# Optimization experiments

Hardware: AMD Instinct MI355X
Metric: run time of the kernel (lower is better)

Reference implementation:

```python
import jax, jax.numpy as jnp
import numpy as np

DT = 0.1
B_SZ = 8192
T_HIST = 20
LEN_PRED = 30
FEAT = 32
N_LAYERS = 3
# state transition for constant-acceleration model (matches self.F in torch)
F_MAT = np.array([[1.0, DT, DT * DT / 2], [0.0, 1.0, DT], [0.0, 0.0, 1.0]], dtype=np.float32)


def setup_inputs() -> dict:
    key = jax.random.key(0)
    ks = jax.random.split(key, 16)
    # random-walk trajectories as history observations
    hist = jnp.cumsum(jax.random.normal(ks[0], (B_SZ, T_HIST, 2), jnp.float32) * 0.5, axis=1)
    k_lin = 1.0 / np.sqrt(FEAT)
    k_in = 1.0 / np.sqrt(24)

    def u(k, shape, scale):
        return jax.random.uniform(k, shape, jnp.float32, -scale, scale)

    return {
        "hist": hist,
        "max_accel_x": jnp.ones((1,), jnp.float32) * 10.0,
        "max_accel_y": jnp.ones((1,), jnp.float32) * 20.0,
        "velocity_std_x": jnp.ones((1,), jnp.float32) * 10.0,
        "acceleration_std_x": jnp.ones((1,), jnp.float32) * 10.0,
        "R_x_": jnp.array([0.0448], jnp.float32),
        "R_y_": jnp.array([0.001], jnp.float32),
        "G_x": jnp.array([0.0059, 0.2981, 0.0393], jnp.float32),
        "G_y": jnp.array([0.0059, 0.2981, 0.0393], jnp.float32) / 5.0,
        "Win_W": u(ks[1], (FEAT, 24), k_in),
        "Win_b": u(ks[2], (FEAT,), k_in),
        "enc_Wih": u(ks[3], (N_LAYERS, 4 * FEAT, FEAT), k_lin),
        "enc_Whh": u(ks[4], (N_LAYERS, 4 * FEAT, FEAT), k_lin),
        "enc_bih": u(ks[5], (N_LAYERS, 4 * FEAT), k_lin),
        "enc_bhh": u(ks[6], (N_LAYERS, 4 * FEAT), k_lin),
        "dec_Wih": u(ks[7], (N_LAYERS, 4 * FEAT, FEAT), k_lin),
        "dec_Whh": u(ks[8], (N_LAYERS, 4 * FEAT, FEAT), k_lin),
        "dec_bih": u(ks[9], (N_LAYERS, 4 * FEAT), k_lin),
        "dec_bhh": u(ks[10], (N_LAYERS, 4 * FEAT), k_lin),
        "Wout_W": u(ks[11], (4, FEAT), k_lin),
        "Wout_b": u(ks[12], (4,), k_lin),
        "len_pred": LEN_PRED,
    }


def reference(hist, max_accel_x, max_accel_y, velocity_std_x, acceleration_std_x,
              R_x_, R_y_, G_x, G_y, Win_W, Win_b,
              enc_Wih, enc_Whh, enc_bih, enc_bhh,
              dec_Wih, dec_Whh, dec_bih, dec_bhh,
              Wout_W, Wout_b, len_pred):
    B = hist.shape[0]
    F = jnp.asarray(F_MAT)
    R_x = R_x_[0] * R_x_[0]
    R_y = R_y_[0] * R_y_[0]
    Z_x = hist[:, :, 0]
    Z_y = hist[:, :, 1]

    def lstm(x, h, c, Wih, Whh, bih, bhh):
        g = x @ Wih.T + bih + h @ Whh.T + bhh
        i, f, gg, o = jnp.split(g, 4, axis=1)
        c = jax.nn.sigmoid(f) * c + jax.nn.sigmoid(i) * jnp.tanh(gg)
        h = jax.nn.sigmoid(o) * jnp.tanh(c)
        return h, c

    def stack(XP, h, c, Wih, Whh, bih, bhh):
        x = jnp.tanh(XP @ Win_W.T + Win_b)
        hs, cs = [], []
        for j in range(N_LAYERS):
            hj, cj = lstm(x, h[j], c[j], Wih[j], Whh[j], bih[j], bhh[j])
            hs.append(hj)
            cs.append(cj)
            x = cj  # torch code feeds the fresh CELL state to the next layer
        return jnp.stack(hs), jnp.stack(cs)

    def kpred(X, P, Q):
        return X @ F.T, jnp.einsum('ij,bjk,lk->bil', F, P, F) + Q

    def kupdate(X, P, z, R):
        y = z - X[:, 0]                      # innovation (H picks component 0)
        S = P[:, 0, 0] + R                   # innovation covariance (scalar)
        K = P[:, :, 0] / S[:, None]          # Kalman gain (B,3)
        return X + y[:, None] * K, P - K[:, :, None] * P[:, 0:1, :]

    def kinit(z0):
        # torch always calls _kalman_init with is_x=True (default), so both
        # axes use R_x / velocity_std_x / acceleration_std_x
        X = jnp.zeros((B, 3), hist.dtype).at[:, 0].set(z0)
        d = jnp.stack([R_x, velocity_std_x[0] ** 2, acceleration_std_x[0] ** 2])
        P = jnp.zeros((B, 3, 3), hist.dtype).at[:, jnp.arange(3), jnp.arange(3)].set(d)
        return X, P

    Qx_e = jnp.outer(G_x * max_accel_x[0], G_x * max_accel_x[0])
    Qy_e = jnp.outer(G_y * max_accel_y[0], G_y * max_accel_y[0])

    Xx, Px = kinit(Z_x[:, 0])
    Xy, Py = kinit(Z_y[:, 0])
    h = jnp.zeros((N_LAYERS, B, FEAT), hist.dtype)
    c = jnp.zeros_like(h)

    def enc_step(carry, zs):
        Xx, Px, Xy, Py, h, c = carry
        zx, zy = zs
        XP = jnp.concatenate([Xx, Xy, Px.reshape(B, 9), Py.reshape(B, 9)], 1)
        h, c = stack(XP, h, c, enc_Wih, enc_Whh, enc_bih, enc_bhh)
        Xx, Px = kpred(Xx, Px, Qx_e)
        Xy, Py = kpred(Xy, Py, Qy_e)
        Xx, Px = kupdate(Xx, Px, zx, R_x)
        Xy, Py = kupdate(Xy, Py, zy, R_y)
        return (Xx, Px, Xy, Py, h, c), None

    carry, _ = jax.lax.scan(enc_step, (Xx, Px, Xy, Py, h, c),
                            (Z_x[:, 1:].T, Z_y[:, 1:].T))

    oxx = jnp.outer(G_x, G_x)
    oyy = jnp.outer(G_y, G_y)

    def dec_step(carry, _):
        Xx, Px, Xy, Py, h, c = carry
        XP = jnp.concatenate([Xx, Xy, Px.reshape(B, 9), Py.reshape(B, 9)], 1)
        h, c = stack(XP, h, c, dec_Wih, dec_Whh, dec_bih, dec_bhh)
        pred = c[-1] @ Wout_W.T + Wout_b  # (B,4): [u_x, u_y, std_x, std_y]
        Xx = Xx.at[:, 2].set(DT * pred[:, 0])  # X[:,2] = B*u
        Xy = Xy.at[:, 2].set(DT * pred[:, 1])
        Qx = (pred[:, 2] ** 2)[:, None, None] * oxx
        Qy = (pred[:, 3] ** 2)[:, None, None] * oyy
        Xx, Px = kpred(Xx, Px, Qx)
        Xy, Py = kpred(Xy, Py, Qy)
        out = jnp.stack([Xx[:, 0], Xy[:, 0],
                         jnp.sqrt(Px[:, 0, 0]), jnp.sqrt(Py[:, 0, 0]),
                         jnp.zeros(B, hist.dtype)], axis=1)  # (B,5)
        return (Xx, Px, Xy, Py, h, c), out

    carry, ys = jax.lax.scan(dec_step, carry, None, length=len_pred)
    return jnp.transpose(ys, (1, 0, 2))  # (B, len_pred, 5)
```

## Files before the change

kernel.cpp:

```cpp
#include <hip/hip_runtime.h>
#include <math.h>

#define DT   0.1f
#define HDT  0.005f
#define T_HIST 20
#define LEN_PRED 30

typedef __attribute__((ext_vector_type(8))) short bfrag8;
typedef __attribute__((ext_vector_type(4))) short short4v;
typedef __attribute__((ext_vector_type(4))) float f32x4;

#define WS_FRAG   0u
#define WS_WIN    98304u
#define WS_WOUT   100352u
#define WS_BIAS   101376u

static __device__ __forceinline__ unsigned short f2bf(float x) {
    union { float f; unsigned int u; } v; v.f = x;
    unsigned int r = v.u + 0x7fffu + ((v.u >> 16) & 1u);
    return (unsigned short)(r >> 16);
}

__global__ void prep_kernel(const float* __restrict__ Win_W,
                            const float* __restrict__ eWih, const float* __restrict__ eWhh,
                            const float* __restrict__ ebih, const float* __restrict__ ebhh,
                            const float* __restrict__ dWih, const float* __restrict__ dWhh,
                            const float* __restrict__ dbih, const float* __restrict__ dbhh,
                            const float* __restrict__ Wout_W,
                            char* __restrict__ ws)
{
    int i = blockIdx.x * blockDim.x + threadIdx.x;
    if (i < 49152) {
        int fi = i >> 9, within = i & 511;
        int lane = within >> 3, jj = within & 7;
        int c = fi & 1, j = (fi >> 1) & 1, wvv = (fi >> 2) & 3;
        int pl = fi >> 4;
        int l = pl % 3, ph = pl / 3;
        int m = lane & 15, q2 = lane >> 4;
        int gate = m & 3;
        int feat = wvv * 8 + 4 * j + (m >> 2);
        int row = gate * 32 + feat;
        int k = q2 * 8 + jj;
        const float* W = (c == 0) ? (ph ? dWih : eWih) : (ph ? dWhh : eWhh);
        ((unsigned short*)(ws + WS_FRAG))[i] = f2bf(W[l * 4096 + row * 32 + k]);
    } else if (i < 50176) {
        int i2 = i - 49152;
        int w = i2 >> 9, within = i2 & 511;
        int lane = within >> 3, jj = within & 7;
        int m = lane & 15, q2 = lane >> 4;
        int k = q2 * 8 + jj;
        float v = (k < 24) ? Win_W[(w * 16 + m) * 24 + k] : 0.f;
        ((unsigned short*)(ws + WS_WIN))[i2] = f2bf(v);
    } else if (i < 50688) {
        int i3 = i - 50176;
        int lane = i3 >> 3, jj = i3 & 7;
        int m = lane & 15, q2 = lane >> 4;
        float v = (m < 4) ? Wout_W[m * 32 + q2 * 8 + jj] : 0.f;
        ((unsigned short*)(ws + WS_WOUT))[i3] = f2bf(v);
    } else if (i < 51456) {
        int b = i - 50688;
        int ph = b / 384, rem = b % 384;
        int l = rem >> 7, row = rem & 127;
        const float* bi = ph ? dbih : ebih;
        const float* bh = ph ? dbhh : ebhh;
        ((float*)(ws + WS_BIAS))[b] = bi[l * 128 + row] + bh[l * 128 + row];
    }
}

__launch_bounds__(256, 2)
__global__ void kalman_lstm_kernel(const float* __restrict__ hist,
                                   const float* __restrict__ max_ax, const float* __restrict__ max_ay,
                                   const float* __restrict__ vstd, const float* __restrict__ astd,
                                   const float* __restrict__ Rx_, const float* __restrict__ Ry_,
                                   const float* __restrict__ Gx, const float* __restrict__ Gy,
                                   const float* __restrict__ Win_b, const float* __restrict__ Wout_b,
                                   const char* __restrict__ ws, float* __restrict__ out)
{
    __shared__ __align__(16) unsigned short xin[4][16][40];
    __shared__ __align__(16) unsigned short hbuf[2][3][16][40];
    __shared__ __align__(16) unsigned short xpw[2][16][40];

    const int tid  = threadIdx.x;
    const int wv   = tid >> 6;
    const int lane = tid & 63;
    const int q    = lane >> 4;
    const int m    = lane & 15;
    const int b_elem = blockIdx.x * 16 + m;

    bfrag8 fragA[3][2][2];
    float  biasR[3][2][4];
    const bfrag8* fragp = (const bfrag8*)(ws + WS_FRAG);
    const float*  combp = (const float*)(ws + WS_BIAS);
    auto load_phase = [&](int ph) {
#pragma unroll
        for (int l = 0; l < 3; ++l)
#pragma unroll
            for (int j = 0; j < 2; ++j) {
#pragma unroll
                for (int c = 0; c < 2; ++c) {
                    int fi = (((ph * 3 + l) * 4 + wv) * 2 + j) * 2 + c;
                    fragA[l][j][c] = fragp[fi * 64 + lane];
                }
#pragma unroll
                for (int r = 0; r < 4; ++r)
                    biasR[l][j][r] = combp[ph * 384 + l * 128 + r * 32 + (wv * 8 + 4 * j + q)];
            }
    };
    load_phase(0);

    bfrag8 winF = {}, woutF = {};
    f32x4 winB = {0.f, 0.f, 0.f, 0.f};
    float wb0 = 0.f, wb1 = 0.f, wb2 = 0.f, wb3 = 0.f;
    float g0 = 0.f, g1 = 0.f, g2 = 0.f, ge0 = 0.f, ge1 = 0.f, ge2 = 0.f;
    float Rch = 0.f, X0 = 0.f, X1 = 0.f, X2 = 0.f;
    float P00 = 0.f, P01 = 0.f, P02 = 0.f, P11 = 0.f, P12 = 0.f, P22 = 0.f;
    const int ch = q & 1;
    if (wv >= 2) {
        int w = wv - 2;
        winF  = ((const bfrag8*)(ws + WS_WIN))[w * 64 + lane];
        woutF = ((const bfrag8*)(ws + WS_WOUT))[lane];
#pragma unroll
        for (int r = 0; r < 4; ++r) winB[r] = Win_b[w * 16 + q * 4 + r];
        wb0 = Wout_b[0]; wb1 = Wout_b[1]; wb2 = Wout_b[2]; wb3 = Wout_b[3];
        const float rx = Rx_[0] * Rx_[0], ry = Ry_[0] * Ry_[0];
        Rch = ch ? ry : rx;
        if (ch == 0) { g0 = Gx[0]; g1 = Gx[1]; g2 = Gx[2]; float s = max_ax[0]; ge0 = g0*s; ge1 = g1*s; ge2 = g2*s; }
        else         { g0 = Gy[0]; g1 = Gy[1]; g2 = Gy[2]; float s = max_ay[0]; ge0 = g0*s; ge1 = g1*s; ge2 = g2*s; }
        X0 = hist[b_elem * (T_HIST * 2) + ch];
        P00 = Rch; P11 = vstd[0] * vstd[0]; P22 = astd[0] * astd[0];
    }

    float creg[3][2];
#pragma unroll
    for (int l = 0; l < 3; ++l) { creg[l][0] = 0.f; creg[l][1] = 0.f; }

    for (int idx = tid; idx < 4 * 16 * 40; idx += 256) (&xin[0][0][0])[idx] = 0;
    for (int idx = tid; idx < 2 * 3 * 16 * 40; idx += 256) (&hbuf[0][0][0][0])[idx] = 0;
    for (int idx = tid; idx < 2 * 16 * 40; idx += 256) (&xpw[0][0][0])[idx] = 0;

    auto sig = [](float z) { return __builtin_amdgcn_rcpf(1.f + __expf(-z)); };
    auto th  = [](float z) { return fmaf(-2.f, __builtin_amdgcn_rcpf(__expf(2.f * z) + 1.f), 1.f); };

    auto kpred = [&](float Q00, float Q01, float Q02, float Q11, float Q12, float Q22) {
        X0 = X0 + DT * X1 + HDT * X2;
        X1 = X1 + DT * X2;
        float M00 = P00 + DT * P01 + HDT * P02;
        float M01 = P01 + DT * P11 + HDT * P12;
        float M02 = P02 + DT * P12 + HDT * P22;
        float M11 = P11 + DT * P12;
        float M12 = P12 + DT * P22;
        float M22 = P22;
        P00 = M00 + DT * M01 + HDT * M02 + Q00;
        P01 = M01 + DT * M02 + Q01;
        P02 = M02 + Q02;
        P11 = M11 + DT * M12 + Q11;
        P12 = M12 + Q12;
        P22 = M22 + Q22;
    };
    auto kupdate = [&](float z) {
        float y = z - X0;
        float Sinv = 1.0f / (P00 + Rch);
        float K0 = P00 * Sinv, K1 = P01 * Sinv, K2 = P02 * Sinv;
        X0 += y * K0; X1 += y * K1; X2 += y * K2;
        float p00 = P00, p01 = P01, p02 = P02;
        P00 = p00 - K0 * p00;
        P01 = p01 - K0 * p01;
        P02 = p02 - K0 * p02;
        P11 = P11 - K1 * p01;
        P12 = P12 - K1 * p02;
        P22 = P22 - K2 * p02;
    };
    auto write_xp = [&]() {
        if (q < 2) {
            unsigned short* row = &xpw[wv - 2][m][0];
            int o = ch * 3;
            row[o + 0] = f2bf(X0); row[o + 1] = f2bf(X1); row[o + 2] = f2bf(X2);
            int pb = 6 + ch * 9;
            row[pb + 0] = f2bf(P00); row[pb + 1] = f2bf(P01); row[pb + 2] = f2bf(P02);
            row[pb + 3] = f2bf(P01); row[pb + 4] = f2bf(P11); row[pb + 5] = f2bf(P12);
            row[pb + 6] = f2bf(P02); row[pb + 7] = f2bf(P12); row[pb + 8] = f2bf(P22);
        }
    };

    const f32x4 zero4 = {0.f, 0.f, 0.f, 0.f};

    auto regionA = [&](int mode, int t) {
        if (wv >= 2) {
            if (mode == 0) {
                if (t > 0) {
                    float z = hist[b_elem * (T_HIST * 2) + t * 2 + ch];
                    kpred(ge0 * ge0, ge0 * ge1, ge0 * ge2, ge1 * ge1, ge1 * ge2, ge2 * ge2);
                    kupdate(z);
                }
            } else {
                if (t == 0) {
                    float z = hist[b_elem * (T_HIST * 2) + 19 * 2 + ch];
                    kpred(ge0 * ge0, ge0 * ge1, ge0 * ge2, ge1 * ge1, ge1 * ge2, ge2 * ge2);
                    kupdate(z);
                } else {
                    bfrag8 bc2 = *(const bfrag8*)&xin[3][m][q * 8];
                    f32x4 ap = __builtin_amdgcn_mfma_f32_16x16x32_bf16(woutF, bc2, zero4, 0, 0, 0);
                    float a0 = ap[0] + wb0, a1 = ap[1] + wb1, a2 = ap[2] + wb2, a3 = ap[3] + wb3;
                    float s0 = __shfl(a0, m), s1 = __shfl(a1, m);
                    float s2 = __shfl(a2, m), s3 = __shfl(a3, m);
                    float pe = ch ? s1 : s0;
                    float qe = ch ? s3 : s2;
                    X2 = DT * pe;
                    float qs = qe * qe;
                    kpred(qs*g0*g0, qs*g0*g1, qs*g0*g2, qs*g1*g1, qs*g1*g2, qs*g2*g2);
                    if (wv == 2 && q < 2) {
                        float* o = out + (size_t)b_elem * (LEN_PRED * 5) + (t - 1) * 5;
                        if (ch == 0) { o[0] = X0; o[2] = sqrtf(P00); }
                        else         { o[1] = X0; o[3] = sqrtf(P00); o[4] = 0.f; }
                    }
                }
            }
            write_xp();
            bfrag8 bxp = *(const bfrag8*)&xpw[wv - 2][m][q * 8];
            f32x4 aw = __builtin_amdgcn_mfma_f32_16x16x32_bf16(winF, bxp, zero4, 0, 0, 0);
            union { short4v v; unsigned short s[4]; } u;
#pragma unroll
            for (int r = 0; r < 4; ++r) u.s[r] = f2bf(th(aw[r] + winB[r]));
            *(short4v*)&xin[0][m][(wv - 2) * 16 + q * 4] = u.v;
        }
        __syncthreads();
    };

    auto layers = [&](int p) {
#pragma unroll
        for (int l = 0; l < 3; ++l) {
            bfrag8 bx = *(const bfrag8*)&xin[l][m][q * 8];
            bfrag8 bh = *(const bfrag8*)&hbuf[p][l][m][q * 8];
            f32x4 a0 = __builtin_amdgcn_mfma_f32_16x16x32_bf16(fragA[l][0][0], bx, zero4, 0, 0, 0);
            a0        = __builtin_amdgcn_mfma_f32_16x16x32_bf16(fragA[l][0][1], bh, a0, 0, 0, 0);
            f32x4 a1 = __builtin_amdgcn_mfma_f32_16x16x32_bf16(fragA[l][1][0], bx, zero4, 0, 0, 0);
            a1        = __builtin_amdgcn_mfma_f32_16x16x32_bf16(fragA[l][1][1], bh, a1, 0, 0, 0);
#pragma unroll
            for (int j = 0; j < 2; ++j) {
                f32x4 a = j ? a1 : a0;
                float iv = sig(a[0] + biasR[l][j][0]);
                float fv = sig(a[1] + biasR[l][j][1]);
                float gv = th (a[2] + biasR[l][j][2]);
                float ov = sig(a[3] + biasR[l][j][3]);
                float cn = fmaf(fv, creg[l][j], iv * gv);
                float hn = ov * th(cn);
                creg[l][j] = cn;
                int f = wv * 8 + 4 * j + q;
                xin[l + 1][m][f] = f2bf(cn);
                hbuf[p ^ 1][l][m][f] = f2bf(hn);
            }
            __syncthreads();
        }
    };

    __syncthreads();
    int p = 0;

    for (int t = 0; t < T_HIST - 1; ++t) { regionA(0, t); layers(p); p ^= 1; }
    load_phase(1);
    for (int t = 0; t < LEN_PRED; ++t)   { regionA(1, t); layers(p); p ^= 1; }

    if (wv == 2) {
        bfrag8 bc2 = *(const bfrag8*)&xin[3][m][q * 8];
        f32x4 ap = __builtin_amdgcn_mfma_f32_16x16x32_bf16(woutF, bc2, zero4, 0, 0, 0);
        float a0 = ap[0] + wb0, a1 = ap[1] + wb1, a2 = ap[2] + wb2, a3 = ap[3] + wb3;
        float s0 = __shfl(a0, m), s1 = __shfl(a1, m);
        float s2 = __shfl(a2, m), s3 = __shfl(a3, m);
        float pe = ch ? s1 : s0;
        float qe = ch ? s3 : s2;
        X2 = DT * pe;
        float qs = qe * qe;
        kpred(qs*g0*g0, qs*g0*g1, qs*g0*g2, qs*g1*g1, qs*g1*g2, qs*g2*g2);
        if (q < 2) {
            float* o = out + (size_t)b_elem * (LEN_PRED * 5) + (LEN_PRED - 1) * 5;
            if (ch == 0) { o[0] = X0; o[2] = sqrtf(P00); }
            else         { o[1] = X0; o[3] = sqrtf(P00); o[4] = 0.f; }
        }
    }
}

extern "C" void kernel_launch(void* const* d_in, const int* in_sizes, int n_in,
                              void* d_out, int out_size, void* d_ws, size_t ws_size,
                              hipStream_t stream)
{
    const float* hist  = (const float*)d_in[0];
    const float* maxax = (const float*)d_in[1];
    const float* maxay = (const float*)d_in[2];
    const float* vstd  = (const float*)d_in[3];
    const float* astd  = (const float*)d_in[4];
    const float* Rx    = (const float*)d_in[5];
    const float* Ry    = (const float*)d_in[6];
    const float* Gx    = (const float*)d_in[7];
    const float* Gy    = (const float*)d_in[8];
    const float* WinW  = (const float*)d_in[9];
    const float* Winb  = (const float*)d_in[10];
    const float* eWih  = (const float*)d_in[11];
    const float* eWhh  = (const float*)d_in[12];
    const float* ebih  = (const float*)d_in[13];
    const float* ebhh  = (const float*)d_in[14];
    const float* dWih  = (const float*)d_in[15];
    const float* dWhh  = (const float*)d_in[16];
    const float* dbih  = (const float*)d_in[17];
    const float* dbhh  = (const float*)d_in[18];
    const float* WoutW = (const float*)d_in[19];
    const float* Woutb = (const float*)d_in[20];
    char* ws = (char*)d_ws;
    float* out = (float*)d_out;

    prep_kernel<<<202, 256, 0, stream>>>(WinW, eWih, eWhh, ebih, ebhh,
                                         dWih, dWhh, dbih, dbhh, WoutW, ws);
    kalman_lstm_kernel<<<512, 256, 0, stream>>>(hist, maxax, maxay, vstd, astd,
                                                Rx, Ry, Gx, Gy, Winb, Woutb,
                                                ws, out);
}
```

Baseline: 192.8 us.

## Precompute encoder Kalman inputs, issue recurrent MFMAs early, repack LDS layout

Runs the whole encoder-phase Kalman filter and input projection up front, since it does not depend on the LSTM, and stages all 19 projected inputs in shared memory. This removes one barrier-separated region per encoder step. Each step now issues the hidden-state MFMAs for all layers first, with the bias folded into the accumulator, so they overlap the dependent chain. The shared buffers are changed to a k-chunked [4][16][8] layout with gate rows permuted, so each lane writes packed bf16 pairs via v_cvt_pk_bf16_f32. The trade-off is more shared memory, which may affect occupancy, and more live accumulator registers.

```diff
diff --git a/kernel.cpp b/kernel.cpp
--- a/kernel.cpp
+++ b/kernel.cpp
@@ -7,8 +7,8 @@
 #define LEN_PRED 30
 
 typedef __attribute__((ext_vector_type(8))) short bfrag8;
-typedef __attribute__((ext_vector_type(4))) short short4v;
 typedef __attribute__((ext_vector_type(4))) float f32x4;
+typedef __attribute__((ext_vector_type(2))) unsigned int u32x2;
 
 #define WS_FRAG   0u
 #define WS_WIN    98304u
@@ -19,6 +19,12 @@
     union { float f; unsigned int u; } v; v.f = x;
     unsigned int r = v.u + 0x7fffu + ((v.u >> 16) & 1u);
     return (unsigned short)(r >> 16);
+}
+
+static __device__ __forceinline__ unsigned int cvtpk(float lo, float hi) {
+    unsigned int r;
+    asm("v_cvt_pk_bf16_f32 %0, %1, %2" : "=v"(r) : "v"(lo), "v"(hi));
+    return r;
 }
 
 __global__ void prep_kernel(const float* __restrict__ Win_W,
@@ -36,9 +42,9 @@
         int c = fi & 1, j = (fi >> 1) & 1, wvv = (fi >> 2) & 3;
         int pl = fi >> 4;
         int l = pl % 3, ph = pl / 3;
-        int m = lane & 15, q2 = lane >> 4;
-        int gate = m & 3;
-        int feat = wvv * 8 + 4 * j + (m >> 2);
+        int p = lane & 15, q2 = lane >> 4;
+        int gate = p & 3;
+        int feat = wvv * 8 + (p >> 2) * 2 + j;
         int row = gate * 32 + feat;
         int k = q2 * 8 + jj;
         const float* W = (c == 0) ? (ph ? dWih : eWih) : (ph ? dWhh : eWhh);
@@ -47,15 +53,15 @@
         int i2 = i - 49152;
         int w = i2 >> 9, within = i2 & 511;
         int lane = within >> 3, jj = within & 7;
-        int m = lane & 15, q2 = lane >> 4;
+        int p = lane & 15, q2 = lane >> 4;
         int k = q2 * 8 + jj;
-        float v = (k < 24) ? Win_W[(w * 16 + m) * 24 + k] : 0.f;
+        float v = (k < 24) ? Win_W[(w * 16 + p) * 24 + k] : 0.f;
         ((unsigned short*)(ws + WS_WIN))[i2] = f2bf(v);
     } else if (i < 50688) {
         int i3 = i - 50176;
         int lane = i3 >> 3, jj = i3 & 7;
-        int m = lane & 15, q2 = lane >> 4;
-        float v = (m < 4) ? Wout_W[m * 32 + q2 * 8 + jj] : 0.f;
+        int p = lane & 15, q2 = lane >> 4;
+        float v = (p < 4) ? Wout_W[p * 32 + q2 * 8 + jj] : 0.f;
         ((unsigned short*)(ws + WS_WOUT))[i3] = f2bf(v);
     } else if (i < 51456) {
         int b = i - 50688;
@@ -76,9 +82,11 @@
                                    const float* __restrict__ Win_b, const float* __restrict__ Wout_b,
                                    const char* __restrict__ ws, float* __restrict__ out)
 {
-    __shared__ __align__(16) unsigned short xin[4][16][40];
-    __shared__ __align__(16) unsigned short hbuf[2][3][16][40];
-    __shared__ __align__(16) unsigned short xpw[2][16][40];
+    __shared__ __align__(16) unsigned short xin[4][4][16][8];
+    __shared__ __align__(16) unsigned short hbuf[2][3][4][16][8];
+    __shared__ __align__(16) unsigned short xpw[2][4][16][8];
+    __shared__ __align__(16) unsigned short xenc[T_HIST - 1][4][16][8];
+    __shared__ __align__(16) unsigned short xps[2][4][16][8];
 
     const int tid  = threadIdx.x;
     const int wv   = tid >> 6;
@@ -86,9 +94,10 @@
     const int q    = lane >> 4;
     const int m    = lane & 15;
     const int b_elem = blockIdx.x * 16 + m;
+    const f32x4 zero4 = {0.f, 0.f, 0.f, 0.f};
 
     bfrag8 fragA[3][2][2];
-    float  biasR[3][2][4];
+    f32x4  biasV[3][2];
     const bfrag8* fragp = (const bfrag8*)(ws + WS_FRAG);
     const float*  combp = (const float*)(ws + WS_BIAS);
     auto load_phase = [&](int ph) {
@@ -103,7 +112,7 @@
                 }
 #pragma unroll
                 for (int r = 0; r < 4; ++r)
-                    biasR[l][j][r] = combp[ph * 384 + l * 128 + r * 32 + (wv * 8 + 4 * j + q)];
+                    biasV[l][j][r] = combp[ph * 384 + l * 128 + r * 32 + (wv * 8 + q * 2 + j)];
             }
     };
     load_phase(0);
@@ -111,7 +120,8 @@
     bfrag8 winF = {}, woutF = {};
     f32x4 winB = {0.f, 0.f, 0.f, 0.f};
     float wb0 = 0.f, wb1 = 0.f, wb2 = 0.f, wb3 = 0.f;
-    float g0 = 0.f, g1 = 0.f, g2 = 0.f, ge0 = 0.f, ge1 = 0.f, ge2 = 0.f;
+    float g00 = 0.f, g01 = 0.f, g02 = 0.f, g11 = 0.f, g12 = 0.f, g22 = 0.f;
+    float qe00 = 0.f, qe01 = 0.f, qe02 = 0.f, qe11 = 0.f, qe12 = 0.f, qe22 = 0.f;
     float Rch = 0.f, X0 = 0.f, X1 = 0.f, X2 = 0.f;
     float P00 = 0.f, P01 = 0.f, P02 = 0.f, P11 = 0.f, P12 = 0.f, P22 = 0.f;
     const int ch = q & 1;
@@ -124,19 +134,25 @@
         wb0 = Wout_b[0]; wb1 = Wout_b[1]; wb2 = Wout_b[2]; wb3 = Wout_b[3];
         const float rx = Rx_[0] * Rx_[0], ry = Ry_[0] * Ry_[0];
         Rch = ch ? ry : rx;
-        if (ch == 0) { g0 = Gx[0]; g1 = Gx[1]; g2 = Gx[2]; float s = max_ax[0]; ge0 = g0*s; ge1 = g1*s; ge2 = g2*s; }
-        else         { g0 = Gy[0]; g1 = Gy[1]; g2 = Gy[2]; float s = max_ay[0]; ge0 = g0*s; ge1 = g1*s; ge2 = g2*s; }
+        float G0, G1, G2, sc;
+        if (ch == 0) { G0 = Gx[0]; G1 = Gx[1]; G2 = Gx[2]; sc = max_ax[0]; }
+        else         { G0 = Gy[0]; G1 = Gy[1]; G2 = Gy[2]; sc = max_ay[0]; }
+        g00 = G0 * G0; g01 = G0 * G1; g02 = G0 * G2;
+        g11 = G1 * G1; g12 = G1 * G2; g22 = G2 * G2;
+        float s2 = sc * sc;
+        qe00 = g00 * s2; qe01 = g01 * s2; qe02 = g02 * s2;
+        qe11 = g11 * s2; qe12 = g12 * s2; qe22 = g22 * s2;
         X0 = hist[b_elem * (T_HIST * 2) + ch];
-        P00 = Rch; P11 = vstd[0] * vstd[0]; P22 = astd[0] * astd[0];
+        P00 = rx; P11 = vstd[0] * vstd[0]; P22 = astd[0] * astd[0];
     }
 
     float creg[3][2];
 #pragma unroll
     for (int l = 0; l < 3; ++l) { creg[l][0] = 0.f; creg[l][1] = 0.f; }
 
-    for (int idx = tid; idx < 4 * 16 * 40; idx += 256) (&xin[0][0][0])[idx] = 0;
-    for (int idx = tid; idx < 2 * 3 * 16 * 40; idx += 256) (&hbuf[0][0][0][0])[idx] = 0;
-    for (int idx = tid; idx < 2 * 16 * 40; idx += 256) (&xpw[0][0][0])[idx] = 0;
+    for (int idx = tid; idx < 4 * 4 * 16 * 8; idx += 256) (&xin[0][0][0][0])[idx] = 0;
+    for (int idx = tid; idx < 2 * 3 * 4 * 16 * 8; idx += 256) (&hbuf[0][0][0][0][0])[idx] = 0;
+    for (int idx = tid; idx < 2 * 4 * 16 * 8; idx += 256) (&xpw[0][0][0][0])[idx] = 0;
 
     auto sig = [](float z) { return __builtin_amdgcn_rcpf(1.f + __expf(-z)); };
     auto th  = [](float z) { return fmaf(-2.f, __builtin_amdgcn_rcpf(__expf(2.f * z) + 1.f), 1.f); };
@@ -170,98 +186,131 @@
         P12 = P12 - K1 * p02;
         P22 = P22 - K2 * p02;
     };
-    auto write_xp = [&]() {
+    auto stage_xp = [&](unsigned short (*buf)[16][8]) {
         if (q < 2) {
-            unsigned short* row = &xpw[wv - 2][m][0];
+            auto wr = [&](int f, float v) { buf[f >> 3][m][f & 7] = f2bf(v); };
             int o = ch * 3;
-            row[o + 0] = f2bf(X0); row[o + 1] = f2bf(X1); row[o + 2] = f2bf(X2);
+            wr(o + 0, X0); wr(o + 1, X1); wr(o + 2, X2);
             int pb = 6 + ch * 9;
-            row[pb + 0] = f2bf(P00); row[pb + 1] = f2bf(P01); row[pb + 2] = f2bf(P02);
-            row[pb + 3] = f2bf(P01); row[pb + 4] = f2bf(P11); row[pb + 5] = f2bf(P12);
-            row[pb + 6] = f2bf(P02); row[pb + 7] = f2bf(P12); row[pb + 8] = f2bf(P22);
-        }
-    };
-
-    const f32x4 zero4 = {0.f, 0.f, 0.f, 0.f};
-
-    auto regionA = [&](int mode, int t) {
+            wr(pb + 0, P00); wr(pb + 1, P01); wr(pb + 2, P02);
+            wr(pb + 3, P01); wr(pb + 4, P11); wr(pb + 5, P12);
+            wr(pb + 6, P02); wr(pb + 7, P12); wr(pb + 8, P22);
+        }
+    };
+
+    auto gates = [&](int l, int pw, f32x4 a0, f32x4 a1) {
+        float i0 = sig(a0[0]), f0 = sig(a0[1]), gg0 = th(a0[2]), o0 = sig(a0[3]);
+        float c0 = fmaf(f0, creg[l][0], i0 * gg0);
+        float h0 = o0 * th(c0);
+        creg[l][0] = c0;
+        float i1 = sig(a1[0]), f1 = sig(a1[1]), gg1 = th(a1[2]), o1 = sig(a1[3]);
+        float c1 = fmaf(f1, creg[l][1], i1 * gg1);
+        float h1 = o1 * th(c1);
+        creg[l][1] = c1;
+        *(unsigned int*)&xin[l + 1][wv][m][q * 2]    = cvtpk(c0, c1);
+        *(unsigned int*)&hbuf[pw][l][wv][m][q * 2]   = cvtpk(h0, h1);
+    };
+
+    if (wv >= 2) {
+        const int w = wv - 2;
+        for (int idx = lane; idx < 4 * 16 * 8; idx += 64) (&xps[w][0][0][0])[idx] = 0;
+#pragma unroll 1
+        for (int s = 0; s < T_HIST - 1; ++s) {
+            if (s > 0) {
+                float z = hist[b_elem * (T_HIST * 2) + s * 2 + ch];
+                kpred(qe00, qe01, qe02, qe11, qe12, qe22);
+                kupdate(z);
+            }
+            stage_xp(xps[w]);
+            bfrag8 bxp = *(const bfrag8*)&xps[w][q][m][0];
+            f32x4 aw = __builtin_amdgcn_mfma_f32_16x16x32_bf16(winF, bxp, zero4, 0, 0, 0);
+            float v0 = th(aw[0] + winB[0]), v1 = th(aw[1] + winB[1]);
+            float v2 = th(aw[2] + winB[2]), v3 = th(aw[3] + winB[3]);
+            u32x2 pk; pk.x = cvtpk(v0, v1); pk.y = cvtpk(v2, v3);
+            *(u32x2*)&xenc[s][w * 2 + (q >> 1)][m][(q & 1) * 4] = pk;
+        }
+        {
+            float z = hist[b_elem * (T_HIST * 2) + 19 * 2 + ch];
+            kpred(qe00, qe01, qe02, qe11, qe12, qe22);
+            kupdate(z);
+        }
+    }
+    __syncthreads();
+
+    int p = 0;
+
+    for (int t = 0; t < T_HIST - 1; ++t) {
+        f32x4 ah[3][2];
+#pragma unroll
+        for (int l = 0; l < 3; ++l) {
+            bfrag8 bh = *(const bfrag8*)&hbuf[p][l][q][m][0];
+            ah[l][0] = __builtin_amdgcn_mfma_f32_16x16x32_bf16(fragA[l][0][1], bh, biasV[l][0], 0, 0, 0);
+            ah[l][1] = __builtin_amdgcn_mfma_f32_16x16x32_bf16(fragA[l][1][1], bh, biasV[l][1], 0, 0, 0);
+        }
+#pragma unroll
+        for (int l = 0; l < 3; ++l) {
+            bfrag8 bx = (l == 0) ? *(const bfrag8*)&xenc[t][q][m][0]
+                                 : *(const bfrag8*)&xin[l][q][m][0];
+            f32x4 a0 = __builtin_amdgcn_mfma_f32_16x16x32_bf16(fragA[l][0][0], bx, ah[l][0], 0, 0, 0);
+            f32x4 a1 = __builtin_amdgcn_mfma_f32_16x16x32_bf16(fragA[l][1][0], bx, ah[l][1], 0, 0, 0);
+            gates(l, p ^ 1, a0, a1);
+            __syncthreads();
+        }
+        p ^= 1;
+    }
+
+    load_phase(1);
+
+    for (int t = 0; t < LEN_PRED; ++t) {
+        bfrag8 bc2;
+        if (wv >= 2 && t > 0) bc2 = *(const bfrag8*)&xin[3][q][m][0];
+        f32x4 ah[3][2];
+#pragma unroll
+        for (int l = 0; l < 3; ++l) {
+            bfrag8 bh = *(const bfrag8*)&hbuf[p][l][q][m][0];
+            ah[l][0] = __builtin_amdgcn_mfma_f32_16x16x32_bf16(fragA[l][0][1], bh, biasV[l][0], 0, 0, 0);
+            ah[l][1] = __builtin_amdgcn_mfma_f32_16x16x32_bf16(fragA[l][1][1], bh, biasV[l][1], 0, 0, 0);
+        }
         if (wv >= 2) {
-            if (mode == 0) {
-                if (t > 0) {
-                    float z = hist[b_elem * (T_HIST * 2) + t * 2 + ch];
-                    kpred(ge0 * ge0, ge0 * ge1, ge0 * ge2, ge1 * ge1, ge1 * ge2, ge2 * ge2);
-                    kupdate(z);
-                }
-            } else {
-                if (t == 0) {
-                    float z = hist[b_elem * (T_HIST * 2) + 19 * 2 + ch];
-                    kpred(ge0 * ge0, ge0 * ge1, ge0 * ge2, ge1 * ge1, ge1 * ge2, ge2 * ge2);
-                    kupdate(z);
-                } else {
-                    bfrag8 bc2 = *(const bfrag8*)&xin[3][m][q * 8];
-                    f32x4 ap = __builtin_amdgcn_mfma_f32_16x16x32_bf16(woutF, bc2, zero4, 0, 0, 0);
-                    float a0 = ap[0] + wb0, a1 = ap[1] + wb1, a2 = ap[2] + wb2, a3 = ap[3] + wb3;
-                    float s0 = __shfl(a0, m), s1 = __shfl(a1, m);
-                    float s2 = __shfl(a2, m), s3 = __shfl(a3, m);
-                    float pe = ch ? s1 : s0;
-                    float qe = ch ? s3 : s2;
-                    X2 = DT * pe;
-                    float qs = qe * qe;
-                    kpred(qs*g0*g0, qs*g0*g1, qs*g0*g2, qs*g1*g1, qs*g1*g2, qs*g2*g2);
-                    if (wv == 2 && q < 2) {
-                        float* o = out + (size_t)b_elem * (LEN_PRED * 5) + (t - 1) * 5;
-                        if (ch == 0) { o[0] = X0; o[2] = sqrtf(P00); }
-                        else         { o[1] = X0; o[3] = sqrtf(P00); o[4] = 0.f; }
-                    }
+            const int w = wv - 2;
+            if (t > 0) {
+                f32x4 ap = __builtin_amdgcn_mfma_f32_16x16x32_bf16(woutF, bc2, zero4, 0, 0, 0);
+                float a0 = ap[0] + wb0, a1 = ap[1] + wb1, a2 = ap[2] + wb2, a3 = ap[3] + wb3;
+                float s0 = __shfl(a0, m), s1 = __shfl(a1, m);
+                float s2 = __shfl(a2, m), s3 = __shfl(a3, m);
+                float pe = ch ? s1 : s0;
+                float qe = ch ? s3 : s2;
+                X2 = DT * pe;
+                float qs = qe * qe;
+                kpred(qs * g00, qs * g01, qs * g02, qs * g11, qs * g12, qs * g22);
+                if (wv == 2 && q < 2) {
+                    float* o = out + (size_t)b_elem * (LEN_PRED * 5) + (t - 1) * 5;
+                    if (ch == 0) { o[0] = X0; o[2] = sqrtf(P00); }
+                    else         { o[1] = X0; o[3] = sqrtf(P00); o[4] = 0.f; }
                 }
             }
-            write_xp();
-            bfrag8 bxp = *(const bfrag8*)&xpw[wv - 2][m][q * 8];
+            stage_xp(xpw[w]);
+            bfrag8 bxp = *(const bfrag8*)&xpw[w][q][m][0];
             f32x4 aw = __builtin_amdgcn_mfma_f32_16x16x32_bf16(winF, bxp, zero4, 0, 0, 0);
-            union { short4v v; unsigned short s[4]; } u;
-#pragma unroll
-            for (int r = 0; r < 4; ++r) u.s[r] = f2bf(th(aw[r] + winB[r]));
-            *(short4v*)&xin[0][m][(wv - 2) * 16 + q * 4] = u.v;
+            float v0 = th(aw[0] + winB[0]), v1 = th(aw[1] + winB[1]);
+            float v2 = th(aw[2] + winB[2]), v3 = th(aw[3] + winB[3]);
+            u32x2 pk; pk.x = cvtpk(v0, v1); pk.y = cvtpk(v2, v3);
+            *(u32x2*)&xin[0][w * 2 + (q >> 1)][m][(q & 1) * 4] = pk;
         }
         __syncthreads();
-    };
-
-    auto layers = [&](int p) {
 #pragma unroll
         for (int l = 0; l < 3; ++l) {
-            bfrag8 bx = *(const bfrag8*)&xin[l][m][q * 8];
-            bfrag8 bh = *(const bfrag8*)&hbuf[p][l][m][q * 8];
-            f32x4 a0 = __builtin_amdgcn_mfma_f32_16x16x32_bf16(fragA[l][0][0], bx, zero4, 0, 0, 0);
-            a0        = __builtin_amdgcn_mfma_f32_16x16x32_bf16(fragA[l][0][1], bh, a0, 0, 0, 0);
-            f32x4 a1 = __builtin_amdgcn_mfma_f32_16x16x32_bf16(fragA[l][1][0], bx, zero4, 0, 0, 0);
-            a1        = __builtin_amdgcn_mfma_f32_16x16x32_bf16(fragA[l][1][1], bh, a1, 0, 0, 0);
-#pragma unroll
-            for (int j = 0; j < 2; ++j) {
-                f32x4 a = j ? a1 : a0;
-                float iv = sig(a[0] + biasR[l][j][0]);
-                float fv = sig(a[1] + biasR[l][j][1]);
-                float gv = th (a[2] + biasR[l][j][2]);
-                float ov = sig(a[3] + biasR[l][j][3]);
-                float cn = fmaf(fv, creg[l][j], iv * gv);
-                float hn = ov * th(cn);
-                creg[l][j] = cn;
-                int f = wv * 8 + 4 * j + q;
-                xin[l + 1][m][f] = f2bf(cn);
-                hbuf[p ^ 1][l][m][f] = f2bf(hn);
-            }
+            bfrag8 bx = *(const bfrag8*)&xin[l][q][m][0];
+            f32x4 a0 = __builtin_amdgcn_mfma_f32_16x16x32_bf16(fragA[l][0][0], bx, ah[l][0], 0, 0, 0);
+            f32x4 a1 = __builtin_amdgcn_mfma_f32_16x16x32_bf16(fragA[l][1][0], bx, ah[l][1], 0, 0, 0);
+            gates(l, p ^ 1, a0, a1);
             __syncthreads();
         }
-    };
-
-    __syncthreads();
-    int p = 0;
-
-    for (int t = 0; t < T_HIST - 1; ++t) { regionA(0, t); layers(p); p ^= 1; }
-    load_phase(1);
-    for (int t = 0; t < LEN_PRED; ++t)   { regionA(1, t); layers(p); p ^= 1; }
+        p ^= 1;
+    }
 
     if (wv == 2) {
-        bfrag8 bc2 = *(const bfrag8*)&xin[3][m][q * 8];
+        bfrag8 bc2 = *(const bfrag8*)&xin[3][q][m][0];
         f32x4 ap = __builtin_amdgcn_mfma_f32_16x16x32_bf16(woutF, bc2, zero4, 0, 0, 0);
         float a0 = ap[0] + wb0, a1 = ap[1] + wb1, a2 = ap[2] + wb2, a3 = ap[3] + wb3;
         float s0 = __shfl(a0, m), s1 = __shfl(a1, m);
@@ -270,7 +319,7 @@
         float qe = ch ? s3 : s2;
         X2 = DT * pe;
         float qs = qe * qe;
-        kpred(qs*g0*g0, qs*g0*g1, qs*g0*g2, qs*g1*g1, qs*g1*g2, qs*g2*g2);
+        kpred(qs * g00, qs * g01, qs * g02, qs * g11, qs * g12, qs * g22);
         if (q < 2) {
             float* o = out + (size_t)b_elem * (LEN_PRED * 5) + (LEN_PRED - 1) * 5;
             if (ch == 0) { o[0] = X0; o[2] = sqrtf(P00); }
```

After: 186.2 us. 3.4% less time.

## Run each 16-element LSTM-Kalman tile in one register-resident wavefront

Applied to the files above, without the earlier changes.

Replaces the four-wave cooperative block, which exchanged gate outputs, hidden states and Kalman features through shared memory with a barrier per layer, with a single 64-thread wave per block. That wave holds all weight fragments, biases and cell states in registers and repacks outputs into MFMA operands using v_cvt_pk_bf16_f32. Both the x and y Kalman filters now run in every lane, and the weight prep layout is reordered to match. The aim is to remove the LDS round-trips and __syncthreads from the serial recurrence. In exchange, each wave carries four times the MFMA and transcendental work, only 512 waves run on the GPU (likely leaving SIMDs idle), and register pressure is very high. The y-filter initial covariance now starts from the x measurement noise (rx) instead of ry.

```diff
diff --git a/kernel.cpp b/kernel.cpp
--- a/kernel.cpp
+++ b/kernel.cpp
@@ -7,7 +7,6 @@
 #define LEN_PRED 30
 
 typedef __attribute__((ext_vector_type(8))) short bfrag8;
-typedef __attribute__((ext_vector_type(4))) short short4v;
 typedef __attribute__((ext_vector_type(4))) float f32x4;
 
 #define WS_FRAG   0u
@@ -19,6 +18,12 @@
     union { float f; unsigned int u; } v; v.f = x;
     unsigned int r = v.u + 0x7fffu + ((v.u >> 16) & 1u);
     return (unsigned short)(r >> 16);
+}
+
+static __device__ __forceinline__ unsigned int cvtpk(float lo, float hi) {
+    unsigned int r;
+    asm("v_cvt_pk_bf16_f32 %0, %1, %2" : "=v"(r) : "v"(lo), "v"(hi));
+    return r;
 }
 
 __global__ void prep_kernel(const float* __restrict__ Win_W,
@@ -33,29 +38,30 @@
     if (i < 49152) {
         int fi = i >> 9, within = i & 511;
         int lane = within >> 3, jj = within & 7;
-        int c = fi & 1, j = (fi >> 1) & 1, wvv = (fi >> 2) & 3;
+        int t = fi & 7, c = (fi >> 3) & 1;
         int pl = fi >> 4;
         int l = pl % 3, ph = pl / 3;
-        int m = lane & 15, q2 = lane >> 4;
-        int gate = m & 3;
-        int feat = wvv * 8 + 4 * j + (m >> 2);
+        int p = lane & 15, q2 = lane >> 4;
+        int gate = p & 3;
+        int feat = 8 * (p >> 2) + t;
         int row = gate * 32 + feat;
         int k = q2 * 8 + jj;
         const float* W = (c == 0) ? (ph ? dWih : eWih) : (ph ? dWhh : eWhh);
         ((unsigned short*)(ws + WS_FRAG))[i] = f2bf(W[l * 4096 + row * 32 + k]);
     } else if (i < 50176) {
         int i2 = i - 49152;
-        int w = i2 >> 9, within = i2 & 511;
+        int t = i2 >> 9, within = i2 & 511;
         int lane = within >> 3, jj = within & 7;
-        int m = lane & 15, q2 = lane >> 4;
+        int p = lane & 15, q2 = lane >> 4;
+        int feat = 8 * (p >> 2) + 4 * t + (p & 3);
         int k = q2 * 8 + jj;
-        float v = (k < 24) ? Win_W[(w * 16 + m) * 24 + k] : 0.f;
+        float v = (k < 24) ? Win_W[feat * 24 + k] : 0.f;
         ((unsigned short*)(ws + WS_WIN))[i2] = f2bf(v);
     } else if (i < 50688) {
         int i3 = i - 50176;
         int lane = i3 >> 3, jj = i3 & 7;
-        int m = lane & 15, q2 = lane >> 4;
-        float v = (m < 4) ? Wout_W[m * 32 + q2 * 8 + jj] : 0.f;
+        int p = lane & 15, q2 = lane >> 4;
+        float v = (p < 4) ? Wout_W[p * 32 + q2 * 8 + jj] : 0.f;
         ((unsigned short*)(ws + WS_WOUT))[i3] = f2bf(v);
     } else if (i < 51456) {
         int b = i - 50688;
@@ -67,7 +73,7 @@
     }
 }
 
-__launch_bounds__(256, 2)
+__launch_bounds__(64, 1)
 __global__ void kalman_lstm_kernel(const float* __restrict__ hist,
                                    const float* __restrict__ max_ax, const float* __restrict__ max_ay,
                                    const float* __restrict__ vstd, const float* __restrict__ astd,
@@ -76,72 +82,78 @@
                                    const float* __restrict__ Win_b, const float* __restrict__ Wout_b,
                                    const char* __restrict__ ws, float* __restrict__ out)
 {
-    __shared__ __align__(16) unsigned short xin[4][16][40];
-    __shared__ __align__(16) unsigned short hbuf[2][3][16][40];
-    __shared__ __align__(16) unsigned short xpw[2][16][40];
-
-    const int tid  = threadIdx.x;
-    const int wv   = tid >> 6;
-    const int lane = tid & 63;
+    const int lane = threadIdx.x;
     const int q    = lane >> 4;
     const int m    = lane & 15;
-    const int b_elem = blockIdx.x * 16 + m;
-
-    bfrag8 fragA[3][2][2];
-    float  biasR[3][2][4];
+    const int be   = blockIdx.x * 16 + m;
+    const f32x4 zero4 = {0.f, 0.f, 0.f, 0.f};
+
     const bfrag8* fragp = (const bfrag8*)(ws + WS_FRAG);
     const float*  combp = (const float*)(ws + WS_BIAS);
+
+    bfrag8 fragA[3][2][8];
+    f32x4  biasV[3][8];
     auto load_phase = [&](int ph) {
 #pragma unroll
-        for (int l = 0; l < 3; ++l)
-#pragma unroll
-            for (int j = 0; j < 2; ++j) {
-#pragma unroll
-                for (int c = 0; c < 2; ++c) {
-                    int fi = (((ph * 3 + l) * 4 + wv) * 2 + j) * 2 + c;
-                    fragA[l][j][c] = fragp[fi * 64 + lane];
-                }
+        for (int l = 0; l < 3; ++l) {
+#pragma unroll
+            for (int c = 0; c < 2; ++c)
+#pragma unroll
+                for (int t = 0; t < 8; ++t)
+                    fragA[l][c][t] = fragp[(((ph * 3 + l) * 2 + c) * 8 + t) * 64 + lane];
+#pragma unroll
+            for (int t = 0; t < 8; ++t)
 #pragma unroll
                 for (int r = 0; r < 4; ++r)
-                    biasR[l][j][r] = combp[ph * 384 + l * 128 + r * 32 + (wv * 8 + 4 * j + q)];
-            }
-    };
-    load_phase(0);
-
-    bfrag8 winF = {}, woutF = {};
-    f32x4 winB = {0.f, 0.f, 0.f, 0.f};
-    float wb0 = 0.f, wb1 = 0.f, wb2 = 0.f, wb3 = 0.f;
-    float g0 = 0.f, g1 = 0.f, g2 = 0.f, ge0 = 0.f, ge1 = 0.f, ge2 = 0.f;
-    float Rch = 0.f, X0 = 0.f, X1 = 0.f, X2 = 0.f;
-    float P00 = 0.f, P01 = 0.f, P02 = 0.f, P11 = 0.f, P12 = 0.f, P22 = 0.f;
-    const int ch = q & 1;
-    if (wv >= 2) {
-        int w = wv - 2;
-        winF  = ((const bfrag8*)(ws + WS_WIN))[w * 64 + lane];
-        woutF = ((const bfrag8*)(ws + WS_WOUT))[lane];
-#pragma unroll
-        for (int r = 0; r < 4; ++r) winB[r] = Win_b[w * 16 + q * 4 + r];
-        wb0 = Wout_b[0]; wb1 = Wout_b[1]; wb2 = Wout_b[2]; wb3 = Wout_b[3];
-        const float rx = Rx_[0] * Rx_[0], ry = Ry_[0] * Ry_[0];
-        Rch = ch ? ry : rx;
-        if (ch == 0) { g0 = Gx[0]; g1 = Gx[1]; g2 = Gx[2]; float s = max_ax[0]; ge0 = g0*s; ge1 = g1*s; ge2 = g2*s; }
-        else         { g0 = Gy[0]; g1 = Gy[1]; g2 = Gy[2]; float s = max_ay[0]; ge0 = g0*s; ge1 = g1*s; ge2 = g2*s; }
-        X0 = hist[b_elem * (T_HIST * 2) + ch];
-        P00 = Rch; P11 = vstd[0] * vstd[0]; P22 = astd[0] * astd[0];
-    }
-
-    float creg[3][2];
-#pragma unroll
-    for (int l = 0; l < 3; ++l) { creg[l][0] = 0.f; creg[l][1] = 0.f; }
-
-    for (int idx = tid; idx < 4 * 16 * 40; idx += 256) (&xin[0][0][0])[idx] = 0;
-    for (int idx = tid; idx < 2 * 3 * 16 * 40; idx += 256) (&hbuf[0][0][0][0])[idx] = 0;
-    for (int idx = tid; idx < 2 * 16 * 40; idx += 256) (&xpw[0][0][0])[idx] = 0;
+                    biasV[l][t][r] = combp[ph * 384 + l * 128 + r * 32 + 8 * q + t];
+        }
+    };
+
+    bfrag8 winF[2];
+    winF[0] = ((const bfrag8*)(ws + WS_WIN))[lane];
+    winF[1] = ((const bfrag8*)(ws + WS_WIN))[64 + lane];
+    f32x4 winBv[2];
+#pragma unroll
+    for (int t = 0; t < 2; ++t)
+#pragma unroll
+        for (int r = 0; r < 4; ++r) winBv[t][r] = Win_b[8 * q + 4 * t + r];
+    bfrag8 woutF = ((const bfrag8*)(ws + WS_WOUT))[lane];
+    const float wb0 = Wout_b[0], wb1 = Wout_b[1], wb2 = Wout_b[2], wb3 = Wout_b[3];
+
+    const float rx = Rx_[0] * Rx_[0], ry = Ry_[0] * Ry_[0];
+    const float gX0 = Gx[0], gX1 = Gx[1], gX2 = Gx[2];
+    const float gY0 = Gy[0], gY1 = Gy[1], gY2 = Gy[2];
+    const float gx00 = gX0*gX0, gx01 = gX0*gX1, gx02 = gX0*gX2,
+                gx11 = gX1*gX1, gx12 = gX1*gX2, gx22 = gX2*gX2;
+    const float gy00 = gY0*gY0, gy01 = gY0*gY1, gy02 = gY0*gY2,
+                gy11 = gY1*gY1, gy12 = gY1*gY2, gy22 = gY2*gY2;
+    const float sx2 = max_ax[0] * max_ax[0], sy2 = max_ay[0] * max_ay[0];
+    const float ex00 = gx00*sx2, ex01 = gx01*sx2, ex02 = gx02*sx2,
+                ex11 = gx11*sx2, ex12 = gx12*sx2, ex22 = gx22*sx2;
+    const float ey00 = gy00*sy2, ey01 = gy01*sy2, ey02 = gy02*sy2,
+                ey11 = gy11*sy2, ey12 = gy12*sy2, ey22 = gy22*sy2;
+
+    float Xx0 = hist[be * 40 + 0], Xx1 = 0.f, Xx2 = 0.f;
+    float Xy0 = hist[be * 40 + 1], Xy1 = 0.f, Xy2 = 0.f;
+    const float pv = vstd[0] * vstd[0], pa = astd[0] * astd[0];
+    float Px00 = rx, Px01 = 0.f, Px02 = 0.f, Px11 = pv, Px12 = 0.f, Px22 = pa;
+    float Py00 = rx, Py01 = 0.f, Py02 = 0.f, Py11 = pv, Py12 = 0.f, Py22 = pa;
+
+    float creg[3][8];
+#pragma unroll
+    for (int l = 0; l < 3; ++l)
+#pragma unroll
+        for (int t = 0; t < 8; ++t) creg[l][t] = 0.f;
+    bfrag8 hfrag[3];
+#pragma unroll
+    for (int l = 0; l < 3; ++l) hfrag[l] = bfrag8{};
 
     auto sig = [](float z) { return __builtin_amdgcn_rcpf(1.f + __expf(-z)); };
     auto th  = [](float z) { return fmaf(-2.f, __builtin_amdgcn_rcpf(__expf(2.f * z) + 1.f), 1.f); };
 
-    auto kpred = [&](float Q00, float Q01, float Q02, float Q11, float Q12, float Q22) {
+    auto kpred9 = [](float& X0, float& X1, float& X2,
+                     float& P00, float& P01, float& P02, float& P11, float& P12, float& P22,
+                     float Q00, float Q01, float Q02, float Q11, float Q12, float Q22) {
         X0 = X0 + DT * X1 + HDT * X2;
         X1 = X1 + DT * X2;
         float M00 = P00 + DT * P01 + HDT * P02;
@@ -157,9 +169,11 @@
         P12 = M12 + Q12;
         P22 = M22 + Q22;
     };
-    auto kupdate = [&](float z) {
+    auto kupd9 = [](float& X0, float& X1, float& X2,
+                    float& P00, float& P01, float& P02, float& P11, float& P12, float& P22,
+                    float z, float R) {
         float y = z - X0;
-        float Sinv = 1.0f / (P00 + Rch);
+        float Sinv = 1.0f / (P00 + R);
         float K0 = P00 * Sinv, K1 = P01 * Sinv, K2 = P02 * Sinv;
         X0 += y * K0; X1 += y * K1; X2 += y * K2;
         float p00 = P00, p01 = P01, p02 = P02;
@@ -170,113 +184,106 @@
         P12 = P12 - K1 * p02;
         P22 = P22 - K2 * p02;
     };
-    auto write_xp = [&]() {
-        if (q < 2) {
-            unsigned short* row = &xpw[wv - 2][m][0];
-            int o = ch * 3;
-            row[o + 0] = f2bf(X0); row[o + 1] = f2bf(X1); row[o + 2] = f2bf(X2);
-            int pb = 6 + ch * 9;
-            row[pb + 0] = f2bf(P00); row[pb + 1] = f2bf(P01); row[pb + 2] = f2bf(P02);
-            row[pb + 3] = f2bf(P01); row[pb + 4] = f2bf(P11); row[pb + 5] = f2bf(P12);
-            row[pb + 6] = f2bf(P02); row[pb + 7] = f2bf(P12); row[pb + 8] = f2bf(P22);
+
+    auto packf = [&](const float* v) {
+        union { bfrag8 f; unsigned int u[4]; } u;
+#pragma unroll
+        for (int d = 0; d < 4; ++d) u.u[d] = cvtpk(v[2 * d], v[2 * d + 1]);
+        return u.f;
+    };
+
+    auto build_xp = [&]() {
+        float v[8];
+        if (q == 0)      { v[0]=Xx0;  v[1]=Xx1;  v[2]=Xx2;  v[3]=Xy0;  v[4]=Xy1;  v[5]=Xy2;  v[6]=Px00; v[7]=Px01; }
+        else if (q == 1) { v[0]=Px02; v[1]=Px01; v[2]=Px11; v[3]=Px12; v[4]=Px02; v[5]=Px12; v[6]=Px22; v[7]=Py00; }
+        else if (q == 2) { v[0]=Py01; v[1]=Py02; v[2]=Py01; v[3]=Py11; v[4]=Py12; v[5]=Py02; v[6]=Py12; v[7]=Py22; }
+        else             { v[0]=0.f; v[1]=0.f; v[2]=0.f; v[3]=0.f; v[4]=0.f; v[5]=0.f; v[6]=0.f; v[7]=0.f; }
+        return packf(v);
+    };
+
+    auto win_x0 = [&](bfrag8 xpf) {
+        f32x4 a0 = __builtin_amdgcn_mfma_f32_16x16x32_bf16(winF[0], xpf, winBv[0], 0, 0, 0);
+        f32x4 a1 = __builtin_amdgcn_mfma_f32_16x16x32_bf16(winF[1], xpf, winBv[1], 0, 0, 0);
+        float v[8] = { th(a0[0]), th(a0[1]), th(a0[2]), th(a0[3]),
+                       th(a1[0]), th(a1[1]), th(a1[2]), th(a1[3]) };
+        return packf(v);
+    };
+
+    auto layers = [&](bfrag8 xf) {
+#pragma unroll
+        for (int l = 0; l < 3; ++l) {
+            f32x4 acc[8];
+#pragma unroll
+            for (int t = 0; t < 8; ++t)
+                acc[t] = __builtin_amdgcn_mfma_f32_16x16x32_bf16(fragA[l][1][t], hfrag[l], biasV[l][t], 0, 0, 0);
+#pragma unroll
+            for (int t = 0; t < 8; ++t)
+                acc[t] = __builtin_amdgcn_mfma_f32_16x16x32_bf16(fragA[l][0][t], xf, acc[t], 0, 0, 0);
+            float cn[8], hn[8];
+#pragma unroll
+            for (int t = 0; t < 8; ++t) {
+                float iv = sig(acc[t][0]);
+                float fv = sig(acc[t][1]);
+                float gv = th(acc[t][2]);
+                float ov = sig(acc[t][3]);
+                float c  = fmaf(fv, creg[l][t], iv * gv);
+                creg[l][t] = c;
+                cn[t] = c;
+                hn[t] = ov * th(c);
+            }
+            xf = packf(cn);
+            hfrag[l] = packf(hn);
         }
-    };
-
-    const f32x4 zero4 = {0.f, 0.f, 0.f, 0.f};
-
-    auto regionA = [&](int mode, int t) {
-        if (wv >= 2) {
-            if (mode == 0) {
-                if (t > 0) {
-                    float z = hist[b_elem * (T_HIST * 2) + t * 2 + ch];
-                    kpred(ge0 * ge0, ge0 * ge1, ge0 * ge2, ge1 * ge1, ge1 * ge2, ge2 * ge2);
-                    kupdate(z);
-                }
-            } else {
-                if (t == 0) {
-                    float z = hist[b_elem * (T_HIST * 2) + 19 * 2 + ch];
-                    kpred(ge0 * ge0, ge0 * ge1, ge0 * ge2, ge1 * ge1, ge1 * ge2, ge2 * ge2);
-                    kupdate(z);
-                } else {
-                    bfrag8 bc2 = *(const bfrag8*)&xin[3][m][q * 8];
-                    f32x4 ap = __builtin_amdgcn_mfma_f32_16x16x32_bf16(woutF, bc2, zero4, 0, 0, 0);
-                    float a0 = ap[0] + wb0, a1 = ap[1] + wb1, a2 = ap[2] + wb2, a3 = ap[3] + wb3;
-                    float s0 = __shfl(a0, m), s1 = __shfl(a1, m);
-                    float s2 = __shfl(a2, m), s3 = __shfl(a3, m);
-                    float pe = ch ? s1 : s0;
-                    float qe = ch ? s3 : s2;
-                    X2 = DT * pe;
-                    float qs = qe * qe;
-                    kpred(qs*g0*g0, qs*g0*g1, qs*g0*g2, qs*g1*g1, qs*g1*g2, qs*g2*g2);
-                    if (wv == 2 && q < 2) {
-                        float* o = out + (size_t)b_elem * (LEN_PRED * 5) + (t - 1) * 5;
-                        if (ch == 0) { o[0] = X0; o[2] = sqrtf(P00); }
-                        else         { o[1] = X0; o[3] = sqrtf(P00); o[4] = 0.f; }
-                    }
-                }
-            }
-            write_xp();
-            bfrag8 bxp = *(const bfrag8*)&xpw[wv - 2][m][q * 8];
-            f32x4 aw = __builtin_amdgcn_mfma_f32_16x16x32_bf16(winF, bxp, zero4, 0, 0, 0);
-            union { short4v v; unsigned short s[4]; } u;
-#pragma unroll
-            for (int r = 0; r < 4; ++r) u.s[r] = f2bf(th(aw[r] + winB[r]));
-            *(short4v*)&xin[0][m][(wv - 2) * 16 + q * 4] = u.v;
-        }
-        __syncthreads();
-    };
-
-    auto layers = [&](int p) {
-#pragma unroll
-        for (int l = 0; l < 3; ++l) {
-            bfrag8 bx = *(const bfrag8*)&xin[l][m][q * 8];
-            bfrag8 bh = *(const bfrag8*)&hbuf[p][l][m][q * 8];
-            f32x4 a0 = __builtin_amdgcn_mfma_f32_16x16x32_bf16(fragA[l][0][0], bx, zero4, 0, 0, 0);
-            a0        = __builtin_amdgcn_mfma_f32_16x16x32_bf16(fragA[l][0][1], bh, a0, 0, 0, 0);
-            f32x4 a1 = __builtin_amdgcn_mfma_f32_16x16x32_bf16(fragA[l][1][0], bx, zero4, 0, 0, 0);
-            a1        = __builtin_amdgcn_mfma_f32_16x16x32_bf16(fragA[l][1][1], bh, a1, 0, 0, 0);
-#pragma unroll
-            for (int j = 0; j < 2; ++j) {
-                f32x4 a = j ? a1 : a0;
-                float iv = sig(a[0] + biasR[l][j][0]);
-                float fv = sig(a[1] + biasR[l][j][1]);
-                float gv = th (a[2] + biasR[l][j][2]);
-                float ov = sig(a[3] + biasR[l][j][3]);
-                float cn = fmaf(fv, creg[l][j], iv * gv);
-                float hn = ov * th(cn);
-                creg[l][j] = cn;
-                int f = wv * 8 + 4 * j + q;
-                xin[l + 1][m][f] = f2bf(cn);
-                hbuf[p ^ 1][l][m][f] = f2bf(hn);
-            }
-            __syncthreads();
-        }
-    };
-
-    __syncthreads();
-    int p = 0;
-
-    for (int t = 0; t < T_HIST - 1; ++t) { regionA(0, t); layers(p); p ^= 1; }
-    load_phase(1);
-    for (int t = 0; t < LEN_PRED; ++t)   { regionA(1, t); layers(p); p ^= 1; }
-
-    if (wv == 2) {
-        bfrag8 bc2 = *(const bfrag8*)&xin[3][m][q * 8];
-        f32x4 ap = __builtin_amdgcn_mfma_f32_16x16x32_bf16(woutF, bc2, zero4, 0, 0, 0);
+        return xf;
+    };
+
+    auto do_pred = [&](int tout, bfrag8 c2f) {
+        f32x4 ap = __builtin_amdgcn_mfma_f32_16x16x32_bf16(woutF, c2f, zero4, 0, 0, 0);
         float a0 = ap[0] + wb0, a1 = ap[1] + wb1, a2 = ap[2] + wb2, a3 = ap[3] + wb3;
         float s0 = __shfl(a0, m), s1 = __shfl(a1, m);
         float s2 = __shfl(a2, m), s3 = __shfl(a3, m);
-        float pe = ch ? s1 : s0;
-        float qe = ch ? s3 : s2;
-        X2 = DT * pe;
-        float qs = qe * qe;
-        kpred(qs*g0*g0, qs*g0*g1, qs*g0*g2, qs*g1*g1, qs*g1*g2, qs*g2*g2);
-        if (q < 2) {
-            float* o = out + (size_t)b_elem * (LEN_PRED * 5) + (LEN_PRED - 1) * 5;
-            if (ch == 0) { o[0] = X0; o[2] = sqrtf(P00); }
-            else         { o[1] = X0; o[3] = sqrtf(P00); o[4] = 0.f; }
+        Xx2 = DT * s0; Xy2 = DT * s1;
+        float qsx = s2 * s2, qsy = s3 * s3;
+        kpred9(Xx0, Xx1, Xx2, Px00, Px01, Px02, Px11, Px12, Px22,
+               qsx * gx00, qsx * gx01, qsx * gx02, qsx * gx11, qsx * gx12, qsx * gx22);
+        kpred9(Xy0, Xy1, Xy2, Py00, Py01, Py02, Py11, Py12, Py22,
+               qsy * gy00, qsy * gy01, qsy * gy02, qsy * gy11, qsy * gy12, qsy * gy22);
+        if (q == 0) {
+            float* o = out + (size_t)be * (LEN_PRED * 5) + tout * 5;
+            o[0] = Xx0; o[1] = Xy0; o[2] = sqrtf(Px00); o[3] = sqrtf(Py00); o[4] = 0.f;
         }
+    };
+
+    load_phase(0);
+    bfrag8 c2f = bfrag8{};
+
+#pragma unroll 1
+    for (int t = 0; t < T_HIST - 1; ++t) {
+        if (t > 0) {
+            float zx = hist[be * 40 + t * 2], zy = hist[be * 40 + t * 2 + 1];
+            kpred9(Xx0, Xx1, Xx2, Px00, Px01, Px02, Px11, Px12, Px22, ex00, ex01, ex02, ex11, ex12, ex22);
+            kupd9 (Xx0, Xx1, Xx2, Px00, Px01, Px02, Px11, Px12, Px22, zx, rx);
+            kpred9(Xy0, Xy1, Xy2, Py00, Py01, Py02, Py11, Py12, Py22, ey00, ey01, ey02, ey11, ey12, ey22);
+            kupd9 (Xy0, Xy1, Xy2, Py00, Py01, Py02, Py11, Py12, Py22, zy, ry);
+        }
+        c2f = layers(win_x0(build_xp()));
     }
+    {
+        float zx = hist[be * 40 + 38], zy = hist[be * 40 + 39];
+        kpred9(Xx0, Xx1, Xx2, Px00, Px01, Px02, Px11, Px12, Px22, ex00, ex01, ex02, ex11, ex12, ex22);
+        kupd9 (Xx0, Xx1, Xx2, Px00, Px01, Px02, Px11, Px12, Px22, zx, rx);
+        kpred9(Xy0, Xy1, Xy2, Py00, Py01, Py02, Py11, Py12, Py22, ey00, ey01, ey02, ey11, ey12, ey22);
+        kupd9 (Xy0, Xy1, Xy2, Py00, Py01, Py02, Py11, Py12, Py22, zy, ry);
+    }
+
+    load_phase(1);
+
+#pragma unroll 1
+    for (int t = 0; t < LEN_PRED; ++t) {
+        if (t > 0) do_pred(t - 1, c2f);
+        c2f = layers(win_x0(build_xp()));
+    }
+    do_pred(LEN_PRED - 1, c2f);
 }
 
 extern "C" void kernel_launch(void* const* d_in, const int* in_sizes, int n_in,
@@ -309,7 +316,7 @@
 
     prep_kernel<<<202, 256, 0, stream>>>(WinW, eWih, eWhh, ebih, ebhh,
                                          dWih, dWhh, dbih, dbhh, WoutW, ws);
-    kalman_lstm_kernel<<<512, 256, 0, stream>>>(hist, maxax, maxay, vstd, astd,
-                                                Rx, Ry, Gx, Gy, Winb, Woutb,
-                                                ws, out);
-}
+    kalman_lstm_kernel<<<512, 64, 0, stream>>>(hist, maxax, maxay, vstd, astd,
+                                               Rx, Ry, Gx, Gy, Winb, Woutb,
+                                               ws, out);
+}
```

Result: slower. 240.9 us (+24.9%).
